# Kernel optimization log

Hardware: AMD Instinct MI355X
Metric: run time of the kernel (lower is better)

## Reference

```python
import jax, jax.numpy as jnp
import numpy as np

DECAY = 0.99
EPS = 1e-05
NUM_EMBEDDINGS = 2048
EMBEDDING_DIM = 512


def setup_inputs() -> dict:
    key = jax.random.key(0)
    k1, k2 = jax.random.split(key)
    z_e = jax.random.normal(k1, (16, 4096, EMBEDDING_DIM), dtype=jnp.float32)
    embedding = jax.random.normal(k2, (NUM_EMBEDDINGS, EMBEDDING_DIM), dtype=jnp.float32)
    cluster_size = jnp.zeros((NUM_EMBEDDINGS,), dtype=jnp.float32)
    embed_avg = embedding  # buffer initialized as a clone of embedding
    return {"z_e": z_e, "embedding": embedding, "cluster_size": cluster_size, "embed_avg": embed_avg}


def reference(z_e, embedding, cluster_size, embed_avg):
    K, D = embedding.shape
    flat = z_e.reshape(-1, D)  # [N, D]
    dist = (jnp.sum(flat * flat, axis=1, keepdims=True)
            - 2.0 * flat @ embedding.T
            + jnp.sum(embedding * embedding, axis=1))
    idx = jnp.argmin(dist, axis=1)  # [N] int
    z_q_raw = embedding[idx].reshape(z_e.shape)

    # EMA cluster statistics (training path). one_hot.T @ flat == segment_sum
    counts = jax.ops.segment_sum(jnp.ones_like(idx, dtype=flat.dtype), idx, num_segments=K)
    embed_sum = jax.ops.segment_sum(flat, idx, num_segments=K)  # [K, D]
    new_cluster_size = DECAY * cluster_size + (1.0 - DECAY) * counts
    new_embed_avg = DECAY * embed_avg + (1.0 - DECAY) * embed_sum
    n = jnp.sum(new_cluster_size)
    cs_smoothed = (new_cluster_size + EPS) / (n + K * EPS) * n
    new_embedding = new_embed_avg / cs_smoothed[:, None]

    # straight-through estimator
    z_q = z_e + jax.lax.stop_gradient(z_q_raw - z_e)
    commit_loss = jnp.mean((jax.lax.stop_gradient(z_e) - z_q) ** 2)
    codebook_loss = jnp.mean((z_e - jax.lax.stop_gradient(z_q)) ** 2)
    vq_loss = codebook_loss + 0.25 * commit_loss
    return (z_q, idx, vq_loss, new_embedding, new_cluster_size, new_embed_avg)
```

## Files before the change

### kernel.cpp

```cpp
#include <hip/hip_runtime.h>

typedef unsigned short ushort_t;
typedef unsigned int u32;
typedef unsigned long long u64;
typedef __attribute__((ext_vector_type(8))) short bf16x8;
typedef __attribute__((ext_vector_type(4))) float f32x4;

#define N_ROWS 65536
#define K_EMB  2048
#define D_DIM  512
#define OFF_ZQ   0
#define OFF_IDX  33554432
#define OFF_LOSS 33619968
#define OFF_EMB  33619969
#define OFF_NCS  34668545
#define OFF_NEA  34670593
#define TAU 1.5f
#define CHUNK 128
#define MAXCHUNK 2560

__device__ __forceinline__ ushort_t f2bf(float f) {
  u32 u = __float_as_uint(f);
  u32 r = (u + 0x7fffu + ((u >> 16) & 1u)) >> 16;
  return (ushort_t)r;
}
__device__ __forceinline__ void glds16(const void* g, void* l) {
  __builtin_amdgcn_global_load_lds((const __attribute__((address_space(1))) u32*)g,
                                   (__attribute__((address_space(3))) u32*)l, 16, 0, 0);
}

#define MERGE4(s1,s2,s3,s4,o1,o2,o3,o4) do {                        \
    u32 x1 = min(s1,o4), x2 = min(s2,o3), x3 = min(s3,o2), x4 = min(s4,o1); \
    u32 t1 = min(x1,x3), t3 = max(x1,x3), t2 = min(x2,x4), t4 = max(x2,x4); \
    s1 = min(t1,t2); s2 = max(t1,t2); s3 = min(t3,t4); s4 = max(t3,t4);     \
  } while (0)

__global__ void prep_z_kernel(const float* __restrict__ ze, ushort_t* __restrict__ xh,
                              float* __restrict__ counts, float* __restrict__ lossws)
{
  int gid = blockIdx.x * 256 + threadIdx.x;
  const float4* zin = (const float4*)ze;
  ushort4* xh4 = (ushort4*)xh;
  for (int g = gid; g < (N_ROWS * D_DIM / 4); g += 8192 * 256) {
    float4 v = zin[g];
    ushort4 h;
    h.x = f2bf(v.x); h.y = f2bf(v.y); h.z = f2bf(v.z); h.w = f2bf(v.w);
    xh4[g] = h;
  }
  if (gid < K_EMB) counts[gid] = 0.0f;
  if (gid == 0) lossws[0] = 0.0f;
}

__global__ void prep_e_kernel(const float* __restrict__ emb, ushort_t* __restrict__ eh,
                              float* __restrict__ enorm)
{
  int w = threadIdx.x >> 6, l = threadIdx.x & 63;
  int k = blockIdx.x * 4 + w;
  const float4* row = (const float4*)(emb + (size_t)k * D_DIM);
  float4 a = row[l * 2], b = row[l * 2 + 1];
  ushort4 h0, h1;
  h0.x = f2bf(a.x); h0.y = f2bf(a.y); h0.z = f2bf(a.z); h0.w = f2bf(a.w);
  h1.x = f2bf(b.x); h1.y = f2bf(b.y); h1.z = f2bf(b.z); h1.w = f2bf(b.w);
  ((ushort4*)(eh + (size_t)k * D_DIM))[l * 2] = h0;
  ((ushort4*)(eh + (size_t)k * D_DIM))[l * 2 + 1] = h1;
  float s = a.x*a.x + a.y*a.y + a.z*a.z + a.w*a.w + b.x*b.x + b.y*b.y + b.z*b.z + b.w*b.w;
  #pragma unroll
  for (int off = 32; off >= 1; off >>= 1) s += __shfl_xor(s, off);
  if (l == 0) enorm[k] = s;
}

__global__ __launch_bounds__(256, 2)
void dist_gemm(const ushort_t* __restrict__ xh, const ushort_t* __restrict__ eh,
               const float* __restrict__ enorm, uint4* __restrict__ list)
{
  __shared__ ushort_t Ah[128 * 64];
  __shared__ ushort_t Bh[128 * 64];
  const int t = threadIdx.x;
  const int w = t >> 6, l = t & 63;
  const int li = l & 15, lg = l >> 4;
  const int row0 = blockIdx.x << 7;
  const int wr = (w >> 1) << 6, wc = (w & 1) << 6;

  u32 cand[16][4];
  #pragma unroll
  for (int mi = 0; mi < 16; ++mi) {
    cand[mi][0] = 0xFFFFFFFFu; cand[mi][1] = 0xFFFFFFFFu;
    cand[mi][2] = 0xFFFFFFFFu; cand[mi][3] = 0xFFFFFFFFu;
  }

  const int Gbase = (w << 6) + l;

  for (int ct = 0; ct < 16; ++ct) {
    const int col0 = ct << 7;
    float en0 = enorm[col0 + wc + 0  + li];
    float en1 = enorm[col0 + wc + 16 + li];
    float en2 = enorm[col0 + wc + 32 + li];
    float en3 = enorm[col0 + wc + 48 + li];

    f32x4 acc[4][4];
    #pragma unroll
    for (int m = 0; m < 4; ++m)
      #pragma unroll
      for (int n = 0; n < 4; ++n) acc[m][n] = (f32x4){0.f, 0.f, 0.f, 0.f};

    for (int kit = 0; kit < 8; ++kit) {
      const int kb = kit << 7;
      #pragma unroll
      for (int i = 0; i < 4; ++i) {
        int G = (i << 8) + Gbase;
        int r = G >> 3, gp = G & 7;
        int cb = gp ^ (r & 7);
        size_t gA = ((size_t)(row0 + r) << 10) + kb + (cb << 4);
        size_t gB = ((size_t)(col0 + r) << 10) + kb + (cb << 4);
        int ld = ((i << 8) + (w << 6)) << 4;
        glds16((const char*)xh + gA, (char*)Ah + ld);
        glds16((const char*)eh + gB, (char*)Bh + ld);
      }
      __syncthreads();
      #pragma unroll
      for (int kblk = 0; kblk < 2; ++kblk) {
        bf16x8 fah[4], fbh[4];
        #pragma unroll
        for (int m = 0; m < 4; ++m) {
          int r = wr + (m << 4) + li;
          int c = (kblk << 2) + lg;
          int off = (r << 7) + ((c ^ (r & 7)) << 4);
          fah[m] = *(const bf16x8*)((const char*)Ah + off);
        }
        #pragma unroll
        for (int n = 0; n < 4; ++n) {
          int r = wc + (n << 4) + li;
          int c = (kblk << 2) + lg;
          int off = (r << 7) + ((c ^ (r & 7)) << 4);
          fbh[n] = *(const bf16x8*)((const char*)Bh + off);
        }
        #pragma unroll
        for (int m = 0; m < 4; ++m)
          #pragma unroll
          for (int n = 0; n < 4; ++n)
            acc[m][n] = __builtin_amdgcn_mfma_f32_16x16x32_bf16(fah[m], fbh[n], acc[m][n], 0, 0, 0);
      }
      __syncthreads();
    }

    const u32 colb = (u32)(col0 + wc + li);
    #pragma unroll
    for (int m = 0; m < 4; ++m)
      #pragma unroll
      for (int i = 0; i < 4; ++i) {
        u32 k0 = (__float_as_uint(fmaf(-2.f, acc[m][0][i], en0)) & 0xFFFFF800u) | colb;
        u32 k1 = (__float_as_uint(fmaf(-2.f, acc[m][1][i], en1)) & 0xFFFFF800u) | (colb + 16u);
        u32 k2 = (__float_as_uint(fmaf(-2.f, acc[m][2][i], en2)) & 0xFFFFF800u) | (colb + 32u);
        u32 k3 = (__float_as_uint(fmaf(-2.f, acc[m][3][i], en3)) & 0xFFFFF800u) | (colb + 48u);
        u32 a = min(k0, k1), b = max(k0, k1);
        u32 c = min(k2, k3), d = max(k2, k3);
        u32 e = min(a, c),  f = max(a, c);
        u32 g = min(b, d),  h = max(b, d);
        u32 q1 = e, q2 = min(f, g), q3 = max(f, g), q4 = h;
        MERGE4(cand[m * 4 + i][0], cand[m * 4 + i][1],
               cand[m * 4 + i][2], cand[m * 4 + i][3], q1, q2, q3, q4);
      }
  }

  #pragma unroll
  for (int mi = 0; mi < 16; ++mi) {
    u32 s1 = cand[mi][0], s2 = cand[mi][1], s3 = cand[mi][2], s4 = cand[mi][3];
    #pragma unroll
    for (int off = 1; off <= 8; off <<= 1) {
      u32 o1 = __shfl_xor(s1, off), o2 = __shfl_xor(s2, off);
      u32 o3 = __shfl_xor(s3, off), o4 = __shfl_xor(s4, off);
      MERGE4(s1, s2, s3, s4, o1, o2, o3, o4);
    }
    cand[mi][0] = s1; cand[mi][1] = s2; cand[mi][2] = s3; cand[mi][3] = s4;
  }

  u32* ex = (u32*)Ah;
  if ((w & 1) == 1 && li == 0) {
    #pragma unroll
    for (int m = 0; m < 4; ++m)
      #pragma unroll
      for (int i = 0; i < 4; ++i) {
        int lrow = wr + (m << 4) + (lg << 2) + i;
        uint4 v;
        v.x = cand[m * 4 + i][0]; v.y = cand[m * 4 + i][1];
        v.z = cand[m * 4 + i][2]; v.w = cand[m * 4 + i][3];
        *(uint4*)&ex[lrow << 2] = v;
      }
  }
  __syncthreads();
  if ((w & 1) == 0 && li == 0) {
    #pragma unroll
    for (int m = 0; m < 4; ++m)
      #pragma unroll
      for (int i = 0; i < 4; ++i) {
        int lrow = wr + (m << 4) + (lg << 2) + i;
        const u32* p = &ex[lrow << 2];
        u32 s1 = cand[m * 4 + i][0], s2 = cand[m * 4 + i][1];
        u32 s3 = cand[m * 4 + i][2], s4 = cand[m * 4 + i][3];
        u32 o1 = p[0], o2 = p[1], o3 = p[2], o4 = p[3];
        MERGE4(s1, s2, s3, s4, o1, o2, o3, o4);
        uint4 v; v.x = s1; v.y = s2; v.z = s3; v.w = s4;
        list[row0 + lrow] = v;
      }
  }
}

__global__ void finalize_kernel(const uint4* __restrict__ list, const float* __restrict__ ze,
                                const float* __restrict__ emb, int* __restrict__ wsidx,
                                float* __restrict__ counts)
{
  int w = threadIdx.x >> 6, l = threadIdx.x & 63;
  int row = blockIdx.x * 4 + w;
  uint4 q = list[row];
  float d1 = __uint_as_float(q.x & 0xFFFFF800u);
  float lim = d1 + TAU;
  bool n2 = (q.y != 0xFFFFFFFFu) && (__uint_as_float(q.y & 0xFFFFF800u) < lim);
  bool n3 = (q.z != 0xFFFFFFFFu) && (__uint_as_float(q.z & 0xFFFFF800u) < lim);
  bool n4 = (q.w != 0xFFFFFFFFu) && (__uint_as_float(q.w & 0xFFFFF800u) < lim);
  int idx;
  if (!(n2 | n3 | n4)) {
    idx = (int)(q.x & 2047u);
  } else {
    double bd = 1e300; int bc = 0x7fffffff;
    const float* xr = ze + (((size_t)row) << 9);
    double xv[8];
    #pragma unroll
    for (int p = 0; p < 8; ++p) xv[p] = (double)xr[(l << 3) + p];
    #pragma unroll
    for (int j = 0; j < 4; ++j) {
      u32 kj = (j == 0) ? q.x : (j == 1) ? q.y : (j == 2) ? q.z : q.w;
      bool ok = (j == 0) || ((kj != 0xFFFFFFFFu) &&
                             (__uint_as_float(kj & 0xFFFFF800u) < lim));
      if (!ok) continue;
      int col = (int)(kj & 2047u);
      const float* er = emb + (((size_t)col) << 9);
      double s = 0.0;
      #pragma unroll
      for (int p = 0; p < 8; ++p) {
        double df = xv[p] - (double)er[(l << 3) + p];
        s += df * df;
      }
      #pragma unroll
      for (int off = 32; off >= 1; off >>= 1) s += __shfl_xor(s, off);
      if (s < bd || (s == bd && col < bc)) { bd = s; bc = col; }
    }
    idx = bc;
  }
  if (l == 0) {
    wsidx[row] = idx;
    atomicAdd(&counts[idx], 1.0f);
  }
}

__global__ void scan_kernel(const float* __restrict__ counts, u32* __restrict__ offsets,
                            u32* __restrict__ cursor, u32* __restrict__ chunkinfo,
                            u32* __restrict__ ntotal)
{
  int t = threadIdx.x;
  int c[8]; int s = 0;
  #pragma unroll
  for (int i = 0; i < 8; ++i) { c[i] = (int)counts[t * 8 + i]; s += c[i]; }
  __shared__ int ts[256];
  ts[t] = s; __syncthreads();
  for (int off = 1; off < 256; off <<= 1) {
    int v = (t >= off) ? ts[t - off] : 0;
    __syncthreads();
    ts[t] += v;
    __syncthreads();
  }
  int run = ts[t] - s;
  int nch[8]; int ns = 0;
  #pragma unroll
  for (int i = 0; i < 8; ++i) {
    offsets[t * 8 + i] = (u32)run;
    cursor[t * 8 + i] = 0;
    run += c[i];
    nch[i] = (c[i] + CHUNK - 1) / CHUNK;
    ns += nch[i];
  }
  __shared__ int ts2[256];
  ts2[t] = ns; __syncthreads();
  for (int off = 1; off < 256; off <<= 1) {
    int v = (t >= off) ? ts2[t - off] : 0;
    __syncthreads();
    ts2[t] += v;
    __syncthreads();
  }
  int cb = ts2[t] - ns;
  #pragma unroll
  for (int i = 0; i < 8; ++i)
    for (int cc = 0; cc < nch[i]; ++cc)
      chunkinfo[cb++] = (u32)(t * 8 + i) | ((u32)cc << 11);
  if (t == 255) *ntotal = (u32)ts2[255];
}

__global__ void scatter_kernel(const int* __restrict__ wsidx, const u32* __restrict__ offsets,
                               u32* __restrict__ cursor, u32* __restrict__ sorted)
{
  int row = blockIdx.x * 256 + threadIdx.x;
  int idx = wsidx[row];
  u32 pos = atomicAdd(&cursor[idx], 1u);
  sorted[offsets[idx] + pos] = (u32)row;
}

__global__ void zesum_kernel(const float* __restrict__ counts, float* __restrict__ esum)
{
  int k = blockIdx.x;
  float c = counts[k];
  if (c == 0.0f || c > (float)CHUNK) {
    esum[((size_t)k << 9) + threadIdx.x] = 0.0f;
    esum[((size_t)k << 9) + 256 + threadIdx.x] = 0.0f;
  }
}

__global__ __launch_bounds__(256)
void zq_seg_kernel(const float* __restrict__ ze, const float* __restrict__ emb,
                   const u32* __restrict__ offsets, const float* __restrict__ counts,
                   const u32* __restrict__ sorted, const u32* __restrict__ chunkinfo,
                   const u32* __restrict__ ntotal, float* __restrict__ o_zq,
                   float* __restrict__ o_idx, float* __restrict__ esum,
                   float* __restrict__ lossws)
{
  int cid = blockIdx.x;
  if (cid >= (int)*ntotal) return;
  u32 rec = chunkinfo[cid];
  int k = rec & 2047, c = (int)(rec >> 11);
  int ctotal = (int)counts[k];
  int base = (int)offsets[k] + c * CHUNK;
  int cnt = min(ctotal - c * CHUNK, CHUNK);
  bool multi = ctotal > CHUNK;
  int t = threadIdx.x, w = t >> 6, l = t & 63;
  __shared__ u32 srow[CHUNK];
  __shared__ float sacc[4 * 512];
  __shared__ float sloss[4];
  if (t < cnt) srow[t] = sorted[base + t];
  __syncthreads();
  const float4* e4 = (const float4*)(emb + ((size_t)k << 9));
  float4 ev0 = e4[l * 2], ev1 = e4[l * 2 + 1];
  float a0x=0,a0y=0,a0z=0,a0w=0,a1x=0,a1y=0,a1z=0,a1w=0;
  float lacc = 0.f;
  for (int r = w; r < cnt; r += 4) {
    int row = (int)srow[r];
    const float4* z4 = (const float4*)(ze + ((size_t)row << 9));
    float4 zv0 = z4[l * 2], zv1 = z4[l * 2 + 1];
    float4 q0, q1;
    q0.x = zv0.x + (ev0.x - zv0.x);
    q0.y = zv0.y + (ev0.y - zv0.y);
    q0.z = zv0.z + (ev0.z - zv0.z);
    q0.w = zv0.w + (ev0.w - zv0.w);
    q1.x = zv1.x + (ev1.x - zv1.x);
    q1.y = zv1.y + (ev1.y - zv1.y);
    q1.z = zv1.z + (ev1.z - zv1.z);
    q1.w = zv1.w + (ev1.w - zv1.w);
    float4* zq4 = (float4*)(o_zq + ((size_t)row << 9));
    zq4[l * 2] = q0; zq4[l * 2 + 1] = q1;
    float dx = zv0.x - q0.x, dy = zv0.y - q0.y, dz = zv0.z - q0.z, dw = zv0.w - q0.w;
    lacc += dx*dx + dy*dy + dz*dz + dw*dw;
    dx = zv1.x - q1.x; dy = zv1.y - q1.y; dz = zv1.z - q1.z; dw = zv1.w - q1.w;
    lacc += dx*dx + dy*dy + dz*dz + dw*dw;
    a0x += zv0.x; a0y += zv0.y; a0z += zv0.z; a0w += zv0.w;
    a1x += zv1.x; a1y += zv1.y; a1z += zv1.z; a1w += zv1.w;
    if (l == 0) o_idx[row] = (float)k;
  }
  #pragma unroll
  for (int off = 32; off >= 1; off >>= 1) lacc += __shfl_xor(lacc, off);
  if (l == 0) sloss[w] = lacc;
  float* sa = sacc + w * 512 + l * 8;
  sa[0]=a0x; sa[1]=a0y; sa[2]=a0z; sa[3]=a0w; sa[4]=a1x; sa[5]=a1y; sa[6]=a1z; sa[7]=a1w;
  __syncthreads();
  #pragma unroll
  for (int j = 0; j < 2; ++j) {
    int col = t * 2 + j;
    float v = sacc[col] + sacc[512 + col] + sacc[1024 + col] + sacc[1536 + col];
    if (multi) atomicAdd(&esum[((size_t)k << 9) + col], v);
    else       esum[((size_t)k << 9) + col] = v;
  }
  if (t == 0) atomicAdd(lossws, sloss[0] + sloss[1] + sloss[2] + sloss[3]);
}

__global__ void d1_kernel(const float* __restrict__ cs, const float* __restrict__ counts,
                          float* __restrict__ o_ncs, float* __restrict__ inv,
                          const float* __restrict__ lossws, float* __restrict__ o_loss)
{
  int t = threadIdx.x;
  float ncs[8]; float s = 0.0f;
  #pragma unroll
  for (int i = 0; i < 8; ++i) {
    int k = t + (i << 8);
    float v = 0.99f * cs[k] + 0.01f * counts[k];
    ncs[i] = v; o_ncs[k] = v; s += v;
  }
  __shared__ float red[256];
  red[t] = s; __syncthreads();
  for (int h = 128; h >= 1; h >>= 1) { if (t < h) red[t] += red[t + h]; __syncthreads(); }
  float n = red[0];
  float denom = n + 2048.0f * 1e-5f;
  #pragma unroll
  for (int i = 0; i < 8; ++i) {
    int k = t + (i << 8);
    float sm = (ncs[i] + 1e-5f) / denom * n;
    inv[k] = 1.0f / sm;
  }
  if (t == 0) o_loss[0] = lossws[0] * 1.25f / 33554432.0f;
}

__global__ void d2_kernel(const float* __restrict__ ea, const float* __restrict__ inv,
                          float* __restrict__ o_emb, float* __restrict__ o_nea)
{
  int gid = blockIdx.x * 256 + threadIdx.x;
  for (int i = gid; i < K_EMB * D_DIM; i += 1024 * 256) {
    float es = o_emb[i];
    float nea = 0.99f * ea[i] + 0.01f * es;
    o_nea[i] = nea;
    o_emb[i] = nea * inv[i >> 9];
  }
}

extern "C" void kernel_launch(void* const* d_in, const int* in_sizes, int n_in,
                              void* d_out, int out_size, void* d_ws, size_t ws_size,
                              hipStream_t stream)
{
  const float* ze  = (const float*)d_in[0];
  const float* emb = (const float*)d_in[1];
  const float* cs  = (const float*)d_in[2];
  const float* ea  = (const float*)d_in[3];
  float* out = (float*)d_out;
  float* o_zq   = out + OFF_ZQ;
  float* o_idx  = out + OFF_IDX;
  float* o_loss = out + OFF_LOSS;
  float* o_emb  = out + OFF_EMB;
  float* o_ncs  = out + OFF_NCS;
  float* o_nea  = out + OFF_NEA;
  ushort_t* xh = (ushort_t*)d_out;
  char* ws = (char*)d_ws;
  ushort_t* ehp = (ushort_t*)ws;
  int* wsidx    = (int*)(ws + 2097152);
  float* counts = (float*)(ws + 2097152 + 262144);
  float* enorm  = counts + 2048;
  float* inv    = enorm + 2048;
  float* lossws = inv + 2048;
  u32* offsets  = (u32*)(lossws + 64);
  u32* cursor   = offsets + 2048;
  u32* sorted   = cursor + 2048;
  u32* chunkinfo= sorted + 65536;
  u32* ntotal   = chunkinfo + MAXCHUNK;
  uint4* list   = (uint4*)(ws + 3145728);

  prep_z_kernel<<<8192, 256, 0, stream>>>(ze, xh, counts, lossws);
  prep_e_kernel<<<512, 256, 0, stream>>>(emb, ehp, enorm);
  dist_gemm<<<512, 256, 0, stream>>>(xh, ehp, enorm, list);
  finalize_kernel<<<16384, 256, 0, stream>>>(list, ze, emb, wsidx, counts);
  scan_kernel<<<1, 256, 0, stream>>>(counts, offsets, cursor, chunkinfo, ntotal);
  scatter_kernel<<<256, 256, 0, stream>>>(wsidx, offsets, cursor, sorted);
  zesum_kernel<<<2048, 256, 0, stream>>>(counts, o_emb);
  zq_seg_kernel<<<MAXCHUNK, 256, 0, stream>>>(ze, emb, offsets, counts, sorted,
                                              chunkinfo, ntotal, o_zq, o_idx, o_emb, lossws);
  d1_kernel<<<1, 256, 0, stream>>>(cs, counts, o_ncs, inv, lossws, o_loss);
  d2_kernel<<<1024, 256, 0, stream>>>(ea, inv, o_emb, o_nea);
}
```

Baseline: 352.3 us.

## Double-buffer LDS and widen dist_gemm to 512 threads with 256-column tiles

Restructures the distance GEMM to use 8 waves per block covering a 128x256 output tile, with LDS double buffering so global-to-LDS loads for the next k-step overlap the MFMA work on the current one. The two syncthreads per k-iteration become one. The top-4 candidate merge across four column waves now goes through LDS. This raises LDS use to 96KB per block and register pressure under launch_bounds(512,2), which may limit occupancy.

```diff
diff --git a/kernel.cpp b/kernel.cpp
--- a/kernel.cpp
+++ b/kernel.cpp
@@ -69,17 +69,18 @@
   if (l == 0) enorm[k] = s;
 }
 
-__global__ __launch_bounds__(256, 2)
+__global__ __launch_bounds__(512, 2)
 void dist_gemm(const ushort_t* __restrict__ xh, const ushort_t* __restrict__ eh,
                const float* __restrict__ enorm, uint4* __restrict__ list)
 {
-  __shared__ ushort_t Ah[128 * 64];
-  __shared__ ushort_t Bh[128 * 64];
+  __shared__ ushort_t Ah[2][128 * 64];
+  __shared__ ushort_t Bh[2][256 * 64];
   const int t = threadIdx.x;
   const int w = t >> 6, l = t & 63;
   const int li = l & 15, lg = l >> 4;
   const int row0 = blockIdx.x << 7;
-  const int wr = (w >> 1) << 6, wc = (w & 1) << 6;
+  const int wrl = (w >> 2) << 6;
+  const int wcl = (w & 3) << 6;
 
   u32 cand[16][4];
   #pragma unroll
@@ -88,78 +89,90 @@
     cand[mi][2] = 0xFFFFFFFFu; cand[mi][3] = 0xFFFFFFFFu;
   }
 
-  const int Gbase = (w << 6) + l;
-
-  for (int ct = 0; ct < 16; ++ct) {
-    const int col0 = ct << 7;
-    float en0 = enorm[col0 + wc + 0  + li];
-    float en1 = enorm[col0 + wc + 16 + li];
-    float en2 = enorm[col0 + wc + 32 + li];
-    float en3 = enorm[col0 + wc + 48 + li];
-
-    f32x4 acc[4][4];
-    #pragma unroll
-    for (int m = 0; m < 4; ++m)
-      #pragma unroll
-      for (int n = 0; n < 4; ++n) acc[m][n] = (f32x4){0.f, 0.f, 0.f, 0.f};
-
-    for (int kit = 0; kit < 8; ++kit) {
-      const int kb = kit << 7;
-      #pragma unroll
-      for (int i = 0; i < 4; ++i) {
-        int G = (i << 8) + Gbase;
-        int r = G >> 3, gp = G & 7;
-        int cb = gp ^ (r & 7);
-        size_t gA = ((size_t)(row0 + r) << 10) + kb + (cb << 4);
-        size_t gB = ((size_t)(col0 + r) << 10) + kb + (cb << 4);
-        int ld = ((i << 8) + (w << 6)) << 4;
-        glds16((const char*)xh + gA, (char*)Ah + ld);
-        glds16((const char*)eh + gB, (char*)Bh + ld);
+  f32x4 acc[4][4];
+  #pragma unroll
+  for (int m = 0; m < 4; ++m)
+    #pragma unroll
+    for (int n = 0; n < 4; ++n) acc[m][n] = (f32x4){0.f, 0.f, 0.f, 0.f};
+
+#define STAGE(buf_, step_) do {                                               \
+    int mct_ = (step_) >> 3, kit_ = (step_) & 7;                              \
+    int kb_ = kit_ << 7;                                                      \
+    _Pragma("unroll")                                                         \
+    for (int i = 0; i < 2; ++i) {                                             \
+      int G = (((i << 3) + w) << 6) + l;                                      \
+      int r = G >> 3, gp = G & 7, cb = gp ^ (r & 7);                          \
+      size_t gA = ((size_t)(row0 + r) << 10) + kb_ + (cb << 4);               \
+      glds16((const char*)xh + gA, (char*)Ah[buf_] + ((((i << 3) + w)) << 10)); \
+    }                                                                         \
+    int col0_ = mct_ << 8;                                                    \
+    _Pragma("unroll")                                                         \
+    for (int i = 0; i < 4; ++i) {                                             \
+      int G = (((i << 3) + w) << 6) + l;                                      \
+      int r = G >> 3, gp = G & 7, cb = gp ^ (r & 7);                          \
+      size_t gB = ((size_t)(col0_ + r) << 10) + kb_ + (cb << 4);              \
+      glds16((const char*)eh + gB, (char*)Bh[buf_] + ((((i << 3) + w)) << 10)); \
+    }                                                                         \
+  } while (0)
+
+  STAGE(0, 0);
+  __syncthreads();
+  int buf = 0;
+
+  for (int step = 0; step < 64; ++step) {
+    if (step != 63) STAGE(buf ^ 1, step + 1);
+    #pragma unroll
+    for (int kblk = 0; kblk < 2; ++kblk) {
+      bf16x8 fah[4], fbh[4];
+      #pragma unroll
+      for (int m = 0; m < 4; ++m) {
+        int r = wrl + (m << 4) + li;
+        int c = (kblk << 2) + lg;
+        int off = (r << 7) + ((c ^ (r & 7)) << 4);
+        fah[m] = *(const bf16x8*)((const char*)Ah[buf] + off);
       }
-      __syncthreads();
-      #pragma unroll
-      for (int kblk = 0; kblk < 2; ++kblk) {
-        bf16x8 fah[4], fbh[4];
+      #pragma unroll
+      for (int n = 0; n < 4; ++n) {
+        int r = wcl + (n << 4) + li;
+        int c = (kblk << 2) + lg;
+        int off = (r << 7) + ((c ^ (r & 7)) << 4);
+        fbh[n] = *(const bf16x8*)((const char*)Bh[buf] + off);
+      }
+      #pragma unroll
+      for (int m = 0; m < 4; ++m)
         #pragma unroll
-        for (int m = 0; m < 4; ++m) {
-          int r = wr + (m << 4) + li;
-          int c = (kblk << 2) + lg;
-          int off = (r << 7) + ((c ^ (r & 7)) << 4);
-          fah[m] = *(const bf16x8*)((const char*)Ah + off);
+        for (int n = 0; n < 4; ++n)
+          acc[m][n] = __builtin_amdgcn_mfma_f32_16x16x32_bf16(fah[m], fbh[n], acc[m][n], 0, 0, 0);
+    }
+
+    if ((step & 7) == 7) {
+      int col0 = (step >> 3) << 8;
+      float en0 = enorm[col0 + wcl + 0  + li];
+      float en1 = enorm[col0 + wcl + 16 + li];
+      float en2 = enorm[col0 + wcl + 32 + li];
+      float en3 = enorm[col0 + wcl + 48 + li];
+      const u32 colb = (u32)(col0 + wcl + li);
+      #pragma unroll
+      for (int m = 0; m < 4; ++m)
+        #pragma unroll
+        for (int i = 0; i < 4; ++i) {
+          u32 k0 = (__float_as_uint(fmaf(-2.f, acc[m][0][i], en0)) & 0xFFFFF800u) | colb;
+          u32 k1 = (__float_as_uint(fmaf(-2.f, acc[m][1][i], en1)) & 0xFFFFF800u) | (colb + 16u);
+          u32 k2 = (__float_as_uint(fmaf(-2.f, acc[m][2][i], en2)) & 0xFFFFF800u) | (colb + 32u);
+          u32 k3 = (__float_as_uint(fmaf(-2.f, acc[m][3][i], en3)) & 0xFFFFF800u) | (colb + 48u);
+          u32 a = min(k0, k1), b = max(k0, k1);
+          u32 c = min(k2, k3), d = max(k2, k3);
+          u32 e = min(a, c),  f = max(a, c);
+          u32 g = min(b, d),  h = max(b, d);
+          u32 q1 = e, q2 = min(f, g), q3 = max(f, g), q4 = h;
+          MERGE4(cand[m * 4 + i][0], cand[m * 4 + i][1],
+                 cand[m * 4 + i][2], cand[m * 4 + i][3], q1, q2, q3, q4);
+          acc[m][0][i] = 0.f; acc[m][1][i] = 0.f;
+          acc[m][2][i] = 0.f; acc[m][3][i] = 0.f;
         }
-        #pragma unroll
-        for (int n = 0; n < 4; ++n) {
-          int r = wc + (n << 4) + li;
-          int c = (kblk << 2) + lg;
-          int off = (r << 7) + ((c ^ (r & 7)) << 4);
-          fbh[n] = *(const bf16x8*)((const char*)Bh + off);
-        }
-        #pragma unroll
-        for (int m = 0; m < 4; ++m)
-          #pragma unroll
-          for (int n = 0; n < 4; ++n)
-            acc[m][n] = __builtin_amdgcn_mfma_f32_16x16x32_bf16(fah[m], fbh[n], acc[m][n], 0, 0, 0);
-      }
-      __syncthreads();
     }
-
-    const u32 colb = (u32)(col0 + wc + li);
-    #pragma unroll
-    for (int m = 0; m < 4; ++m)
-      #pragma unroll
-      for (int i = 0; i < 4; ++i) {
-        u32 k0 = (__float_as_uint(fmaf(-2.f, acc[m][0][i], en0)) & 0xFFFFF800u) | colb;
-        u32 k1 = (__float_as_uint(fmaf(-2.f, acc[m][1][i], en1)) & 0xFFFFF800u) | (colb + 16u);
-        u32 k2 = (__float_as_uint(fmaf(-2.f, acc[m][2][i], en2)) & 0xFFFFF800u) | (colb + 32u);
-        u32 k3 = (__float_as_uint(fmaf(-2.f, acc[m][3][i], en3)) & 0xFFFFF800u) | (colb + 48u);
-        u32 a = min(k0, k1), b = max(k0, k1);
-        u32 c = min(k2, k3), d = max(k2, k3);
-        u32 e = min(a, c),  f = max(a, c);
-        u32 g = min(b, d),  h = max(b, d);
-        u32 q1 = e, q2 = min(f, g), q3 = max(f, g), q4 = h;
-        MERGE4(cand[m * 4 + i][0], cand[m * 4 + i][1],
-               cand[m * 4 + i][2], cand[m * 4 + i][3], q1, q2, q3, q4);
-      }
+    __syncthreads();
+    buf ^= 1;
   }
 
   #pragma unroll
@@ -174,35 +187,38 @@
     cand[mi][0] = s1; cand[mi][1] = s2; cand[mi][2] = s3; cand[mi][3] = s4;
   }
 
-  u32* ex = (u32*)Ah;
-  if ((w & 1) == 1 && li == 0) {
+  uint4* ex = (uint4*)Ah;
+  if ((w & 3) != 0 && li == 0) {
     #pragma unroll
     for (int m = 0; m < 4; ++m)
       #pragma unroll
       for (int i = 0; i < 4; ++i) {
-        int lrow = wr + (m << 4) + (lg << 2) + i;
+        int lrow = wrl + (m << 4) + (lg << 2) + i;
         uint4 v;
         v.x = cand[m * 4 + i][0]; v.y = cand[m * 4 + i][1];
         v.z = cand[m * 4 + i][2]; v.w = cand[m * 4 + i][3];
-        *(uint4*)&ex[lrow << 2] = v;
+        ex[(lrow << 2) + (w & 3)] = v;
       }
   }
   __syncthreads();
-  if ((w & 1) == 0 && li == 0) {
+  if ((w & 3) == 0 && li == 0) {
     #pragma unroll
     for (int m = 0; m < 4; ++m)
       #pragma unroll
       for (int i = 0; i < 4; ++i) {
-        int lrow = wr + (m << 4) + (lg << 2) + i;
-        const u32* p = &ex[lrow << 2];
+        int lrow = wrl + (m << 4) + (lg << 2) + i;
         u32 s1 = cand[m * 4 + i][0], s2 = cand[m * 4 + i][1];
         u32 s3 = cand[m * 4 + i][2], s4 = cand[m * 4 + i][3];
-        u32 o1 = p[0], o2 = p[1], o3 = p[2], o4 = p[3];
-        MERGE4(s1, s2, s3, s4, o1, o2, o3, o4);
+        #pragma unroll
+        for (int cw = 1; cw < 4; ++cw) {
+          uint4 o = ex[(lrow << 2) + cw];
+          MERGE4(s1, s2, s3, s4, o.x, o.y, o.z, o.w);
+        }
         uint4 v; v.x = s1; v.y = s2; v.z = s3; v.w = s4;
         list[row0 + lrow] = v;
       }
   }
+#undef STAGE
 }
 
 __global__ void finalize_kernel(const uint4* __restrict__ list, const float* __restrict__ ze,
@@ -448,7 +464,7 @@
 
   prep_z_kernel<<<8192, 256, 0, stream>>>(ze, xh, counts, lossws);
   prep_e_kernel<<<512, 256, 0, stream>>>(emb, ehp, enorm);
-  dist_gemm<<<512, 256, 0, stream>>>(xh, ehp, enorm, list);
+  dist_gemm<<<512, 512, 0, stream>>>(xh, ehp, enorm, list);
   finalize_kernel<<<16384, 256, 0, stream>>>(list, ze, emb, wsidx, counts);
   scan_kernel<<<1, 256, 0, stream>>>(counts, offsets, cursor, chunkinfo, ntotal);
   scatter_kernel<<<256, 256, 0, stream>>>(wsidx, offsets, cursor, sorted);
```

Result: slower. 392.1 us (+11.3%).

## Split distance GEMM codebook columns across two blocks and merge candidates in finalize

Applied to the files above, without the earlier changes.

The distance GEMM grid doubles, and each block covers half of the codebook columns for its 128 rows. Each half writes its own top-4 candidate list, and finalize merges the 8 candidates, refining with fp64 only when more than one falls within the tolerance. Launch bounds rise to 4 blocks per SM, which caps registers for the large candidate array and may cause spills. The candidate list moves into an unused region of the output buffer, and a barrier is added before shared memory is reused for the exchange.

```diff
diff --git a/kernel.cpp b/kernel.cpp
--- a/kernel.cpp
+++ b/kernel.cpp
@@ -69,7 +69,7 @@
   if (l == 0) enorm[k] = s;
 }
 
-__global__ __launch_bounds__(256, 2)
+__global__ __launch_bounds__(256, 4)
 void dist_gemm(const ushort_t* __restrict__ xh, const ushort_t* __restrict__ eh,
                const float* __restrict__ enorm, uint4* __restrict__ list)
 {
@@ -78,7 +78,9 @@
   const int t = threadIdx.x;
   const int w = t >> 6, l = t & 63;
   const int li = l & 15, lg = l >> 4;
-  const int row0 = blockIdx.x << 7;
+  const int bx = blockIdx.x;
+  const int row0 = (bx >> 1) << 7;
+  const int half = bx & 1;
   const int wr = (w >> 1) << 6, wc = (w & 1) << 6;
 
   u32 cand[16][4];
@@ -90,8 +92,8 @@
 
   const int Gbase = (w << 6) + l;
 
-  for (int ct = 0; ct < 16; ++ct) {
-    const int col0 = ct << 7;
+  for (int ct8 = 0; ct8 < 8; ++ct8) {
+    const int col0 = ((half << 3) + ct8) << 7;
     float en0 = enorm[col0 + wc + 0  + li];
     float en1 = enorm[col0 + wc + 16 + li];
     float en2 = enorm[col0 + wc + 32 + li];
@@ -175,6 +177,7 @@
   }
 
   u32* ex = (u32*)Ah;
+  __syncthreads();
   if ((w & 1) == 1 && li == 0) {
     #pragma unroll
     for (int m = 0; m < 4; ++m)
@@ -200,7 +203,7 @@
         u32 o1 = p[0], o2 = p[1], o3 = p[2], o4 = p[3];
         MERGE4(s1, s2, s3, s4, o1, o2, o3, o4);
         uint4 v; v.x = s1; v.y = s2; v.z = s3; v.w = s4;
-        list[row0 + lrow] = v;
+        list[((size_t)(row0 + lrow) << 1) + half] = v;
       }
   }
 }
@@ -211,15 +214,21 @@
 {
   int w = threadIdx.x >> 6, l = threadIdx.x & 63;
   int row = blockIdx.x * 4 + w;
-  uint4 q = list[row];
-  float d1 = __uint_as_float(q.x & 0xFFFFF800u);
+  uint4 qa = list[(size_t)row << 1];
+  uint4 qb = list[((size_t)row << 1) + 1];
+  u32 ecand[8] = {qa.x, qa.y, qa.z, qa.w, qb.x, qb.y, qb.z, qb.w};
+  u32 m = min(min(min(ecand[0], ecand[1]), min(ecand[2], ecand[3])),
+              min(min(ecand[4], ecand[5]), min(ecand[6], ecand[7])));
+  float d1 = __uint_as_float(m & 0xFFFFF800u);
   float lim = d1 + TAU;
-  bool n2 = (q.y != 0xFFFFFFFFu) && (__uint_as_float(q.y & 0xFFFFF800u) < lim);
-  bool n3 = (q.z != 0xFFFFFFFFu) && (__uint_as_float(q.z & 0xFFFFF800u) < lim);
-  bool n4 = (q.w != 0xFFFFFFFFu) && (__uint_as_float(q.w & 0xFFFFF800u) < lim);
+  int nq = 0;
+  #pragma unroll
+  for (int j = 0; j < 8; ++j)
+    nq += (ecand[j] != 0xFFFFFFFFu &&
+           __uint_as_float(ecand[j] & 0xFFFFF800u) < lim) ? 1 : 0;
   int idx;
-  if (!(n2 | n3 | n4)) {
-    idx = (int)(q.x & 2047u);
+  if (nq <= 1) {
+    idx = (int)(m & 2047u);
   } else {
     double bd = 1e300; int bc = 0x7fffffff;
     const float* xr = ze + (((size_t)row) << 9);
@@ -227,11 +236,10 @@
     #pragma unroll
     for (int p = 0; p < 8; ++p) xv[p] = (double)xr[(l << 3) + p];
     #pragma unroll
-    for (int j = 0; j < 4; ++j) {
-      u32 kj = (j == 0) ? q.x : (j == 1) ? q.y : (j == 2) ? q.z : q.w;
-      bool ok = (j == 0) || ((kj != 0xFFFFFFFFu) &&
-                             (__uint_as_float(kj & 0xFFFFF800u) < lim));
-      if (!ok) continue;
+    for (int j = 0; j < 8; ++j) {
+      u32 kj = ecand[j];
+      if (kj == 0xFFFFFFFFu) continue;
+      if (!(__uint_as_float(kj & 0xFFFFF800u) < lim)) continue;
       int col = (int)(kj & 2047u);
       const float* er = emb + (((size_t)col) << 9);
       double s = 0.0;
@@ -432,6 +440,7 @@
   float* o_ncs  = out + OFF_NCS;
   float* o_nea  = out + OFF_NEA;
   ushort_t* xh = (ushort_t*)d_out;
+  uint4* list  = (uint4*)(out + 16777216);
   char* ws = (char*)d_ws;
   ushort_t* ehp = (ushort_t*)ws;
   int* wsidx    = (int*)(ws + 2097152);
@@ -444,11 +453,10 @@
   u32* sorted   = cursor + 2048;
   u32* chunkinfo= sorted + 65536;
   u32* ntotal   = chunkinfo + MAXCHUNK;
-  uint4* list   = (uint4*)(ws + 3145728);
 
   prep_z_kernel<<<8192, 256, 0, stream>>>(ze, xh, counts, lossws);
   prep_e_kernel<<<512, 256, 0, stream>>>(emb, ehp, enorm);
-  dist_gemm<<<512, 256, 0, stream>>>(xh, ehp, enorm, list);
+  dist_gemm<<<1024, 256, 0, stream>>>(xh, ehp, enorm, list);
   finalize_kernel<<<16384, 256, 0, stream>>>(list, ze, emb, wsidx, counts);
   scan_kernel<<<1, 256, 0, stream>>>(counts, offsets, cursor, chunkinfo, ntotal);
   scatter_kernel<<<256, 256, 0, stream>>>(wsidx, offsets, cursor, sorted);
```

New measurement: 692.1 us. 1.96x slower.

## Double-buffer distance GEMM LDS tiles and merge prep kernels into one launch

Applied to the files above, without the earlier changes.

The distance GEMM now uses two LDS buffers and prefetches the next k-slice with global_load_lds while computing the current one. The column-tile and k loops are flattened into a single 128-step loop, and the top-4 candidate merge runs every eighth step. This cuts one barrier per step and overlaps load latency with MFMA work, at the cost of doubling LDS use to 64 KB per block, which may limit the two-blocks-per-CU occupancy target. The two prep kernels are also fused into one launch to save a kernel launch.

```diff
diff --git a/kernel.cpp b/kernel.cpp
--- a/kernel.cpp
+++ b/kernel.cpp
@@ -35,46 +35,48 @@
     s1 = min(t1,t2); s2 = max(t1,t2); s3 = min(t3,t4); s4 = max(t3,t4);     \
   } while (0)
 
-__global__ void prep_z_kernel(const float* __restrict__ ze, ushort_t* __restrict__ xh,
-                              float* __restrict__ counts, float* __restrict__ lossws)
-{
-  int gid = blockIdx.x * 256 + threadIdx.x;
-  const float4* zin = (const float4*)ze;
-  ushort4* xh4 = (ushort4*)xh;
-  for (int g = gid; g < (N_ROWS * D_DIM / 4); g += 8192 * 256) {
-    float4 v = zin[g];
-    ushort4 h;
-    h.x = f2bf(v.x); h.y = f2bf(v.y); h.z = f2bf(v.z); h.w = f2bf(v.w);
-    xh4[g] = h;
-  }
-  if (gid < K_EMB) counts[gid] = 0.0f;
-  if (gid == 0) lossws[0] = 0.0f;
-}
-
-__global__ void prep_e_kernel(const float* __restrict__ emb, ushort_t* __restrict__ eh,
-                              float* __restrict__ enorm)
-{
-  int w = threadIdx.x >> 6, l = threadIdx.x & 63;
-  int k = blockIdx.x * 4 + w;
-  const float4* row = (const float4*)(emb + (size_t)k * D_DIM);
-  float4 a = row[l * 2], b = row[l * 2 + 1];
-  ushort4 h0, h1;
-  h0.x = f2bf(a.x); h0.y = f2bf(a.y); h0.z = f2bf(a.z); h0.w = f2bf(a.w);
-  h1.x = f2bf(b.x); h1.y = f2bf(b.y); h1.z = f2bf(b.z); h1.w = f2bf(b.w);
-  ((ushort4*)(eh + (size_t)k * D_DIM))[l * 2] = h0;
-  ((ushort4*)(eh + (size_t)k * D_DIM))[l * 2 + 1] = h1;
-  float s = a.x*a.x + a.y*a.y + a.z*a.z + a.w*a.w + b.x*b.x + b.y*b.y + b.z*b.z + b.w*b.w;
-  #pragma unroll
-  for (int off = 32; off >= 1; off >>= 1) s += __shfl_xor(s, off);
-  if (l == 0) enorm[k] = s;
+__global__ void prep_kernel(const float* __restrict__ ze, const float* __restrict__ emb,
+                            ushort_t* __restrict__ xh, ushort_t* __restrict__ eh,
+                            float* __restrict__ enorm, float* __restrict__ counts,
+                            float* __restrict__ lossws)
+{
+  int bx = blockIdx.x;
+  int t = threadIdx.x;
+  if (bx < 512) {
+    int w = t >> 6, l = t & 63;
+    int k = bx * 4 + w;
+    const float4* row = (const float4*)(emb + (size_t)k * D_DIM);
+    float4 a = row[l * 2], b = row[l * 2 + 1];
+    ushort4 h0, h1;
+    h0.x = f2bf(a.x); h0.y = f2bf(a.y); h0.z = f2bf(a.z); h0.w = f2bf(a.w);
+    h1.x = f2bf(b.x); h1.y = f2bf(b.y); h1.z = f2bf(b.z); h1.w = f2bf(b.w);
+    ((ushort4*)(eh + (size_t)k * D_DIM))[l * 2] = h0;
+    ((ushort4*)(eh + (size_t)k * D_DIM))[l * 2 + 1] = h1;
+    float s = a.x*a.x + a.y*a.y + a.z*a.z + a.w*a.w + b.x*b.x + b.y*b.y + b.z*b.z + b.w*b.w;
+    #pragma unroll
+    for (int off = 32; off >= 1; off >>= 1) s += __shfl_xor(s, off);
+    if (l == 0) enorm[k] = s;
+  } else {
+    int gid = (bx - 512) * 256 + t;
+    const float4* zin = (const float4*)ze;
+    ushort4* xh4 = (ushort4*)xh;
+    for (int g = gid; g < (N_ROWS * D_DIM / 4); g += 8192 * 256) {
+      float4 v = zin[g];
+      ushort4 h;
+      h.x = f2bf(v.x); h.y = f2bf(v.y); h.z = f2bf(v.z); h.w = f2bf(v.w);
+      xh4[g] = h;
+    }
+    if (gid < K_EMB) counts[gid] = 0.0f;
+    if (gid == 0) lossws[0] = 0.0f;
+  }
 }
 
 __global__ __launch_bounds__(256, 2)
 void dist_gemm(const ushort_t* __restrict__ xh, const ushort_t* __restrict__ eh,
                const float* __restrict__ enorm, uint4* __restrict__ list)
 {
-  __shared__ ushort_t Ah[128 * 64];
-  __shared__ ushort_t Bh[128 * 64];
+  __shared__ ushort_t Ah[2][128 * 64];
+  __shared__ ushort_t Bh[2][128 * 64];
   const int t = threadIdx.x;
   const int w = t >> 6, l = t & 63;
   const int li = l & 15, lg = l >> 4;
@@ -88,79 +90,95 @@
     cand[mi][2] = 0xFFFFFFFFu; cand[mi][3] = 0xFFFFFFFFu;
   }
 
+  f32x4 acc[4][4];
+  #pragma unroll
+  for (int m = 0; m < 4; ++m)
+    #pragma unroll
+    for (int n = 0; n < 4; ++n) acc[m][n] = (f32x4){0.f, 0.f, 0.f, 0.f};
+
   const int Gbase = (w << 6) + l;
 
-  for (int ct = 0; ct < 16; ++ct) {
-    const int col0 = ct << 7;
-    float en0 = enorm[col0 + wc + 0  + li];
-    float en1 = enorm[col0 + wc + 16 + li];
-    float en2 = enorm[col0 + wc + 32 + li];
-    float en3 = enorm[col0 + wc + 48 + li];
-
-    f32x4 acc[4][4];
-    #pragma unroll
-    for (int m = 0; m < 4; ++m)
-      #pragma unroll
-      for (int n = 0; n < 4; ++n) acc[m][n] = (f32x4){0.f, 0.f, 0.f, 0.f};
-
-    for (int kit = 0; kit < 8; ++kit) {
-      const int kb = kit << 7;
-      #pragma unroll
-      for (int i = 0; i < 4; ++i) {
-        int G = (i << 8) + Gbase;
-        int r = G >> 3, gp = G & 7;
-        int cb = gp ^ (r & 7);
-        size_t gA = ((size_t)(row0 + r) << 10) + kb + (cb << 4);
-        size_t gB = ((size_t)(col0 + r) << 10) + kb + (cb << 4);
-        int ld = ((i << 8) + (w << 6)) << 4;
-        glds16((const char*)xh + gA, (char*)Ah + ld);
-        glds16((const char*)eh + gB, (char*)Bh + ld);
+#define STAGE(buf_, s_) do {                                                   \
+    int kb_ = ((s_) & 7) << 7;                                                 \
+    int c0_ = ((s_) >> 3) << 7;                                                \
+    _Pragma("unroll")                                                          \
+    for (int i = 0; i < 4; ++i) {                                              \
+      int G = (i << 8) + Gbase;                           \
+      int r = G >> 3, gp = G & 7;                                              \
+      int cb = gp ^ (r & 7);                          \
+      size_t gA = ((size_t)(row0 + r) << 10) + kb_ + (cb << 4);                \
+      size_t gB = ((size_t)(c0_ + r) << 10) + kb_ + (cb << 4);                 \
+      int ld = ((i << 8) + (w << 6)) << 4;              \
+      glds16((const char*)xh + gA, (char*)Ah[buf_] + ld);                      \
+      glds16((const char*)eh + gB, (char*)Bh[buf_] + ld);                      \
+    }                                                                          \
+  } while (0)
+
+  STAGE(0, 0);
+  __syncthreads();
+  int buf = 0;
+  float en0 = 0.f, en1 = 0.f, en2 = 0.f, en3 = 0.f;
+
+  for (int s = 0; s < 128; ++s) {
+    if ((s & 7) == 0) {
+      int col0 = (s >> 3) << 7;
+      en0 = enorm[col0 + wc + 0  + li];
+      en1 = enorm[col0 + wc + 16 + li];
+      en2 = enorm[col0 + wc + 32 + li];
+      en3 = enorm[col0 + wc + 48 + li];
+    }
+    if (s != 127) STAGE(buf ^ 1, s + 1);
+
+    #pragma unroll
+    for (int kblk = 0; kblk < 2; ++kblk) {
+      bf16x8 fah[4], fbh[4];
+      #pragma unroll
+      for (int m = 0; m < 4; ++m) {
+        int r = wr + (m << 4) + li;
+        int c = (kblk << 2) + lg;
+        int off = (r << 7) + ((c ^ (r & 7)) << 4);
+        fah[m] = *(const bf16x8*)((const char*)Ah[buf] + off);
       }
-      __syncthreads();
-      #pragma unroll
-      for (int kblk = 0; kblk < 2; ++kblk) {
-        bf16x8 fah[4], fbh[4];
+      #pragma unroll
+      for (int n = 0; n < 4; ++n) {
+        int r = wc + (n << 4) + li;
+        int c = (kblk << 2) + lg;
+        int off = (r << 7) + ((c ^ (r & 7)) << 4);
+        fbh[n] = *(const bf16x8*)((const char*)Bh[buf] + off);
+      }
+      #pragma unroll
+      for (int m = 0; m < 4; ++m)
         #pragma unroll
-        for (int m = 0; m < 4; ++m) {
-          int r = wr + (m << 4) + li;
-          int c = (kblk << 2) + lg;
-          int off = (r << 7) + ((c ^ (r & 7)) << 4);
-          fah[m] = *(const bf16x8*)((const char*)Ah + off);
+        for (int n = 0; n < 4; ++n)
+          acc[m][n] = __builtin_amdgcn_mfma_f32_16x16x32_bf16(fah[m], fbh[n], acc[m][n], 0, 0, 0);
+    }
+
+    if ((s & 7) == 7) {
+      int col0 = (s >> 3) << 7;
+      const u32 colb = (u32)(col0 + wc + li);
+      #pragma unroll
+      for (int m = 0; m < 4; ++m)
+        #pragma unroll
+        for (int i = 0; i < 4; ++i) {
+          u32 k0 = (__float_as_uint(fmaf(-2.f, acc[m][0][i], en0)) & 0xFFFFF800u) | colb;
+          u32 k1 = (__float_as_uint(fmaf(-2.f, acc[m][1][i], en1)) & 0xFFFFF800u) | (colb + 16u);
+          u32 k2 = (__float_as_uint(fmaf(-2.f, acc[m][2][i], en2)) & 0xFFFFF800u) | (colb + 32u);
+          u32 k3 = (__float_as_uint(fmaf(-2.f, acc[m][3][i], en3)) & 0xFFFFF800u) | (colb + 48u);
+          u32 a = min(k0, k1), b = max(k0, k1);
+          u32 c = min(k2, k3), d = max(k2, k3);
+          u32 e = min(a, c),  f = max(a, c);
+          u32 g = min(b, d),  h = max(b, d);
+          u32 q1 = e, q2 = min(f, g), q3 = max(f, g), q4 = h;
+          MERGE4(cand[m * 4 + i][0], cand[m * 4 + i][1],
+                 cand[m * 4 + i][2], cand[m * 4 + i][3], q1, q2, q3, q4);
+          acc[m][0][i] = 0.f; acc[m][1][i] = 0.f;
+          acc[m][2][i] = 0.f; acc[m][3][i] = 0.f;
         }
-        #pragma unroll
-        for (int n = 0; n < 4; ++n) {
-          int r = wc + (n << 4) + li;
-          int c = (kblk << 2) + lg;
-          int off = (r << 7) + ((c ^ (r & 7)) << 4);
-          fbh[n] = *(const bf16x8*)((const char*)Bh + off);
-        }
-        #pragma unroll
-        for (int m = 0; m < 4; ++m)
-          #pragma unroll
-          for (int n = 0; n < 4; ++n)
-            acc[m][n] = __builtin_amdgcn_mfma_f32_16x16x32_bf16(fah[m], fbh[n], acc[m][n], 0, 0, 0);
-      }
-      __syncthreads();
-    }
-
-    const u32 colb = (u32)(col0 + wc + li);
-    #pragma unroll
-    for (int m = 0; m < 4; ++m)
-      #pragma unroll
-      for (int i = 0; i < 4; ++i) {
-        u32 k0 = (__float_as_uint(fmaf(-2.f, acc[m][0][i], en0)) & 0xFFFFF800u) | colb;
-        u32 k1 = (__float_as_uint(fmaf(-2.f, acc[m][1][i], en1)) & 0xFFFFF800u) | (colb + 16u);
-        u32 k2 = (__float_as_uint(fmaf(-2.f, acc[m][2][i], en2)) & 0xFFFFF800u) | (colb + 32u);
-        u32 k3 = (__float_as_uint(fmaf(-2.f, acc[m][3][i], en3)) & 0xFFFFF800u) | (colb + 48u);
-        u32 a = min(k0, k1), b = max(k0, k1);
-        u32 c = min(k2, k3), d = max(k2, k3);
-        u32 e = min(a, c),  f = max(a, c);
-        u32 g = min(b, d),  h = max(b, d);
-        u32 q1 = e, q2 = min(f, g), q3 = max(f, g), q4 = h;
-        MERGE4(cand[m * 4 + i][0], cand[m * 4 + i][1],
-               cand[m * 4 + i][2], cand[m * 4 + i][3], q1, q2, q3, q4);
-      }
-  }
+    }
+    __syncthreads();
+    buf ^= 1;
+  }
+#undef STAGE
 
   #pragma unroll
   for (int mi = 0; mi < 16; ++mi) {
@@ -446,8 +464,7 @@
   u32* ntotal   = chunkinfo + MAXCHUNK;
   uint4* list   = (uint4*)(ws + 3145728);
 
-  prep_z_kernel<<<8192, 256, 0, stream>>>(ze, xh, counts, lossws);
-  prep_e_kernel<<<512, 256, 0, stream>>>(emb, ehp, enorm);
+  prep_kernel<<<8704, 256, 0, stream>>>(ze, emb, xh, ehp, enorm, counts, lossws);
   dist_gemm<<<512, 256, 0, stream>>>(xh, ehp, enorm, list);
   finalize_kernel<<<16384, 256, 0, stream>>>(list, ze, emb, wsidx, counts);
   scan_kernel<<<1, 256, 0, stream>>>(counts, offsets, cursor, chunkinfo, ntotal);
```

Result: faster. 343.7 us (-2.5%).
